# Kernel tuning notes

Measured on AMD Instinct MI355X. Metric: run time of the kernel, lower is better.

## Reference

```python
import jax, jax.numpy as jnp
import numpy as np

DEPTH = 6
N_INTERNAL = 2 ** DEPTH - 1  # 63
N_LEAVES = 2 ** DEPTH        # 64


def _tree_paths(depth):
    """Precompute, for each leaf, its `depth` ancestor internal-node indices and
    whether the path goes right at each ancestor (static heap-indexing of the tree)."""
    n_internal = 2 ** depth - 1
    n_leaves = 2 ** depth
    anc = np.zeros((n_leaves, depth), dtype=np.int32)
    right = np.zeros((n_leaves, depth), dtype=bool)
    for leaf in range(n_leaves):
        node = leaf + n_internal
        for d in range(depth):
            parent = (node - 1) // 2
            anc[leaf, d] = parent
            right[leaf, d] = (node % 2 == 0)
            node = parent
    return jnp.asarray(anc), jnp.asarray(right)

_ANC, _RIGHT = _tree_paths(DEPTH)


def setup_inputs() -> dict:
    key = jax.random.key(0)
    k = jax.random.split(key, 6)
    B, F, T, C = 8192, 256, 32, 100
    return {
        "x": jax.random.normal(k[0], (B, F), dtype=jnp.float32),
        "split_weights": jax.random.normal(k[1], (T, N_INTERNAL, F), dtype=jnp.float32) * 0.05,
        "split_bias": jax.random.normal(k[2], (T, N_INTERNAL), dtype=jnp.float32) * 0.05,
        "leaf_logits": jax.random.normal(k[3], (T, N_LEAVES, C), dtype=jnp.float32),
        "tree_weights": jax.random.normal(k[4], (T,), dtype=jnp.float32),
        "log_temperature": jnp.zeros((), dtype=jnp.float32),
    }


def reference(x, split_weights, split_bias, leaf_logits, tree_weights, log_temperature):
    # temperature = exp(log_temperature).clamp(0.1, 5.0)
    temp = jnp.clip(jnp.exp(log_temperature), 0.1, 5.0)
    # split probabilities for all trees at once: [T, B, N_INTERNAL]
    logits = jnp.einsum('bf,tnf->tbn', x, split_weights) + split_bias[:, None, :]
    split_probs = jax.nn.sigmoid(logits / temp)
    # gather each leaf's ancestor probs: [T, B, L, D]; right -> p, left -> 1-p
    g = split_probs[:, :, _ANC]
    leaf_probs = jnp.prod(jnp.where(_RIGHT, g, 1.0 - g), axis=-1)  # [T, B, L]
    # per-leaf class distributions: [T, L, C]
    leaf_class_probs = jax.nn.softmax(leaf_logits / temp, axis=-1)
    outputs = jnp.einsum('tbl,tlc->tbc', leaf_probs, leaf_class_probs)  # [T, B, C]
    weights = jax.nn.softmax(tree_weights, axis=0)  # [T]
    return jnp.einsum('t,tbc->bc', weights, outputs)  # [B, C]
```

## Files before the change

### kernel.cpp

```cpp
#include <hip/hip_runtime.h>
#include <math.h>

#define B_  8192
#define F_  256
#define T_  32
#define NI_ 63
#define NL_ 64
#define C_  100
#define K2_ (T_*NL_)
#define NG  4
#define TPG 8

typedef unsigned short u16;
typedef __attribute__((ext_vector_type(8))) short bf16x8;
typedef __attribute__((ext_vector_type(4))) float f32x4;
typedef __attribute__((ext_vector_type(8))) unsigned short u16x8;

__device__ __forceinline__ u16 f2bf(float f) {
    unsigned int u = __float_as_uint(f);
    u += 0x7fffu + ((u >> 16) & 1u);
    return (u16)(u >> 16);
}
__device__ __forceinline__ float bf2f(u16 u) {
    return __uint_as_float(((unsigned int)u) << 16);
}

__device__ __forceinline__ void gl16(const void* g, void* l) {
    __builtin_amdgcn_global_load_lds(
        (const __attribute__((address_space(1))) unsigned int*)g,
        (__attribute__((address_space(3))) unsigned int*)l,
        16, 0, 0);
}

#define WSB_SWB   0
#define WSB_LCPT  (T_*32*64*8*2)
#define WSB_XB    (WSB_LCPT + T_*8*112*8*2)
#define WSB_PART  ((size_t)WSB_XB + (size_t)B_*F_*2)
#define WSB_ATOM  WSB_PART
#define WSB_STORE (WSB_PART + (size_t)NG*B_*112*2)

#define SWBLK  (T_*64*32/256)
#define XBLK   (B_*F_/2048)
#define LCPBLK (T_*NL_/256)
#define ZBLK   (B_*C_/256)

__device__ __forceinline__ void cvt8(const float* __restrict__ s, u16* __restrict__ d, int i) {
    const float4* p = (const float4*)(s + i);
    float4 v0 = p[0], v1 = p[1];
    u16x8 o;
    o[0] = f2bf(v0.x); o[1] = f2bf(v0.y); o[2] = f2bf(v0.z); o[3] = f2bf(v0.w);
    o[4] = f2bf(v1.x); o[5] = f2bf(v1.y); o[6] = f2bf(v1.z); o[7] = f2bf(v1.w);
    *(u16x8*)(d + i) = o;
}

__global__ void k_prep(const float* __restrict__ sw, const float* __restrict__ x,
                       const float* __restrict__ ll, const float* __restrict__ tw,
                       const float* __restrict__ logT,
                       u16* __restrict__ swb, u16* __restrict__ xb,
                       u16* __restrict__ lcpT, float* __restrict__ out) {
    int blk = blockIdx.x, tid = threadIdx.x;
    if (blk < SWBLK) {
        int gid = blk * 256 + tid;
        int k8 = gid & 31;
        int n  = (gid >> 5) & 63;
        int t  = gid >> 11;
        u16x8 o;
        if (n < NI_) {
            const float4* p = (const float4*)(sw + ((size_t)(t * NI_ + n)) * F_ + k8 * 8);
            float4 v0 = p[0], v1 = p[1];
            o[0] = f2bf(v0.x); o[1] = f2bf(v0.y); o[2] = f2bf(v0.z); o[3] = f2bf(v0.w);
            o[4] = f2bf(v1.x); o[5] = f2bf(v1.y); o[6] = f2bf(v1.z); o[7] = f2bf(v1.w);
        } else {
            o = (u16x8){0,0,0,0,0,0,0,0};
        }
        *(u16x8*)(swb + (((size_t)t * 32 + k8) * 64 + n) * 8) = o;
        return;
    }
    blk -= SWBLK;
    if (blk < XBLK) { cvt8(x, xb, blk * 2048 + tid * 8); return; }
    blk -= XBLK;
    if (blk >= LCPBLK) {
        out[(blk - LCPBLK) * 256 + tid] = 0.f;
        return;
    }
    int idx = blk * 256 + tid;
    int t = idx >> 6;
    int l = idx & 63;
    int o = l >> 3, jj = l & 7;
    float temp = __expf(logT[0]);
    temp = fminf(fmaxf(temp, 0.1f), 5.0f);
    float invt = 1.0f / temp;

    float m = -1e30f;
    for (int j = 0; j < T_; ++j) m = fmaxf(m, tw[j]);
    float s = 0.f;
    for (int j = 0; j < T_; ++j) s += __expf(tw[j] - m);
    float wt = __expf(tw[t] - m) / s;

    const float* row = ll + (size_t)idx * C_;
    float m2 = -1e30f;
    for (int c = 0; c < C_; ++c) m2 = fmaxf(m2, row[c]);
    float s2 = 0.f;
    for (int c = 0; c < C_; ++c) s2 += __expf((row[c] - m2) * invt);
    float sc = wt / s2;
    u16* base = lcpT + (size_t)t * (8 * 112 * 8);
    for (int c = 0; c < C_; ++c)
        base[(o * 112 + c) * 8 + jj] = f2bf(sc * __expf((row[c] - m2) * invt));
    for (int c = C_; c < 112; ++c)
        base[(o * 112 + c) * 8 + jj] = 0;
}

__device__ __forceinline__ void stage_tree(const u16* __restrict__ swb,
                                           const u16* __restrict__ lcpT,
                                           u16* swsD, u16* lcpD,
                                           int t, int w, int lane) {
    const char* gsw = (const char*)(swb + (size_t)t * (32 * 64 * 8));
    char* lsw = (char*)swsD;
    #pragma unroll
    for (int r = 0; r < 4; ++r)
        gl16(gsw + r * 8192 + w * 1024 + lane * 16,
             lsw + r * 8192 + w * 1024);
    const char* glc = (const char*)(lcpT + (size_t)t * (8 * 112 * 8));
    char* llc = (char*)lcpD;
    gl16(glc + w * 1024 + lane * 16, llc + w * 1024);
    if (w < 6)
        gl16(glc + 8192 + w * 1024 + lane * 16, llc + 8192 + w * 1024);
}

__global__ __launch_bounds__(512, 2)
void k_fused(const u16* __restrict__ xb, const u16* __restrict__ swb,
             const float* __restrict__ sb, const float* __restrict__ logT,
             const u16* __restrict__ lcpT, void* __restrict__ dst, int storeMode) {
    __shared__ __attribute__((aligned(16))) u16 swS[2][32 * 64 * 8];
    __shared__ __attribute__((aligned(16))) u16 lcpS[2][8 * 112 * 8];
    __shared__ float slog[8][16][66];
    int tid  = threadIdx.x;
    int w    = tid >> 6;
    int lane = tid & 63;
    int col  = lane & 15;
    int quad = lane >> 4;
    int mb   = blockIdx.x * 128 + w * 16;
    int tg   = blockIdx.y;

    float temp = __expf(logT[0]);
    temp = fminf(fmaxf(temp, 0.1f), 5.0f);
    float invt = 1.0f / temp;

    bf16x8 afr[8];
    #pragma unroll
    for (int ks = 0; ks < 8; ++ks)
        afr[ks] = *(const bf16x8*)(xb + (size_t)(mb + col) * F_ + ks * 32 + quad * 8);

    stage_tree(swb, lcpT, swS[0], lcpS[0], tg * TPG, w, lane);

    f32x4 accO[7];
    #pragma unroll
    for (int i = 0; i < 7; ++i) accO[i] = (f32x4){0.f, 0.f, 0.f, 0.f};

    int cur = 0;
    #pragma unroll 1
    for (int ti = 0; ti < TPG; ++ti) {
        int t = tg * TPG + ti;

        asm volatile("s_waitcnt vmcnt(0)" ::: "memory");
        __syncthreads();

        if (ti + 1 < TPG)
            stage_tree(swb, lcpT, swS[cur ^ 1], lcpS[cur ^ 1], t + 1, w, lane);

        const u16* sws  = swS[cur];
        const u16* lcps = lcpS[cur];

        f32x4 acc[4];
        #pragma unroll
        for (int i = 0; i < 4; ++i) acc[i] = (f32x4){0.f, 0.f, 0.f, 0.f};
        #pragma unroll
        for (int ks = 0; ks < 8; ++ks) {
            #pragma unroll
            for (int nt = 0; nt < 4; ++nt) {
                int n  = nt * 16 + col;
                int ne = n > 62 ? 62 : n;
                bf16x8 bfr = *(const bf16x8*)&sws[((ks * 4 + quad) * 64 + ne) * 8];
                acc[nt] = __builtin_amdgcn_mfma_f32_16x16x32_bf16(afr[ks], bfr, acc[nt], 0, 0, 0);
            }
        }

        asm volatile("s_waitcnt lgkmcnt(0)" ::: "memory");
        #pragma unroll
        for (int nt = 0; nt < 4; ++nt) {
            int n = nt * 16 + col;
            float bias = (n < NI_) ? sb[t * NI_ + n] : 0.f;
            #pragma unroll
            for (int r = 0; r < 4; ++r) {
                float lg = (acc[nt][r] + bias) * invt;
                slog[w][quad * 4 + r][n] = 1.0f / (1.0f + __expf(-lg));
            }
        }
        asm volatile("s_waitcnt lgkmcnt(0)" ::: "memory");

        bf16x8 af0, af1;
        #pragma unroll
        for (int grp = 0; grp < 2; ++grp) {
            int s = (grp ? 11 : 7) + quad;
            float pref = 1.0f;
            int node = s;
            #pragma unroll
            for (int d = 0; d < 3; ++d) {
                int par = (node - 1) >> 1;
                float g = slog[w][col][par];
                pref = (node & 1) ? (pref - pref * g) : (pref * g);
                node = par;
            }
            float gs  = slog[w][col][s];
            float gl  = slog[w][col][2 * s + 1];
            float gr  = slog[w][col][2 * s + 2];
            float g00 = slog[w][col][4 * s + 3];
            float g01 = slog[w][col][4 * s + 4];
            float g10 = slog[w][col][4 * s + 5];
            float g11 = slog[w][col][4 * s + 6];
            #pragma unroll
            for (int j = 0; j < 8; ++j) {
                const int b2 = (j >> 2) & 1, b1 = (j >> 1) & 1, b0 = j & 1;
                float f3 = b2 ? gs : 1.0f - gs;
                float c1 = b2 ? gr : gl;
                float f4 = b1 ? c1 : 1.0f - c1;
                float c2 = b2 ? (b1 ? g11 : g10) : (b1 ? g01 : g00);
                float f5 = b0 ? c2 : 1.0f - c2;
                float p  = pref * f3 * f4 * f5;
                if (grp == 0) af0[j] = (short)f2bf(p);
                else          af1[j] = (short)f2bf(p);
            }
        }

        #pragma unroll
        for (int nt = 0; nt < 7; ++nt) {
            int n = nt * 16 + col;
            bf16x8 lb0 = *(const bf16x8*)&lcps[(quad * 112 + n) * 8];
            bf16x8 lb1 = *(const bf16x8*)&lcps[((4 + quad) * 112 + n) * 8];
            accO[nt] = __builtin_amdgcn_mfma_f32_16x16x32_bf16(af0, lb0, accO[nt], 0, 0, 0);
            accO[nt] = __builtin_amdgcn_mfma_f32_16x16x32_bf16(af1, lb1, accO[nt], 0, 0, 0);
        }

        cur ^= 1;
    }

    if (storeMode) {
        u16* pp = (u16*)dst + (size_t)tg * B_ * 112;
        #pragma unroll
        for (int nt = 0; nt < 7; ++nt) {
            int c = nt * 16 + col;
            #pragma unroll
            for (int r = 0; r < 4; ++r) {
                int b = mb + quad * 4 + r;
                pp[(size_t)b * 112 + c] = f2bf(accO[nt][r]);
            }
        }
    } else {
        float* od = (float*)dst;
        #pragma unroll
        for (int nt = 0; nt < 7; ++nt) {
            int c = nt * 16 + col;
            if (c < C_) {
                #pragma unroll
                for (int r = 0; r < 4; ++r) {
                    int b = mb + quad * 4 + r;
                    atomicAdd(&od[(size_t)b * C_ + c], accO[nt][r]);
                }
            }
        }
    }
}

__global__ void k_red(const u16* __restrict__ part, float* __restrict__ out) {
    int idx = blockIdx.x * 256 + threadIdx.x;
    int b = idx / 112, c = idx - b * 112;
    if (c < C_) {
        float s = 0.f;
        #pragma unroll
        for (int tg = 0; tg < NG; ++tg)
            s += bf2f(part[((size_t)tg * B_ + b) * 112 + c]);
        out[(size_t)b * C_ + c] = s;
    }
}

__global__ void k_zf(float* __restrict__ out, int n) {
    int i = blockIdx.x * 256 + threadIdx.x;
    if (i < n) out[i] = 0.f;
}

__global__ void k_mono(const float* __restrict__ x, const float* __restrict__ sw,
                       const float* __restrict__ sb, const float* __restrict__ ll,
                       const float* __restrict__ tw, const float* __restrict__ logT,
                       float* __restrict__ outg) {
    __shared__ float slcp[NL_ * C_];
    int tid = threadIdx.x;
    int b = blockIdx.x * 256 + tid;

    float temp = __expf(logT[0]);
    temp = fminf(fmaxf(temp, 0.1f), 5.0f);
    float invt = 1.0f / temp;

    float m = -1e30f;
    for (int j = 0; j < T_; ++j) m = fmaxf(m, tw[j]);
    float sden = 0.f;
    for (int j = 0; j < T_; ++j) sden += __expf(tw[j] - m);

    float acc[C_];
    #pragma unroll
    for (int c = 0; c < C_; ++c) acc[c] = 0.f;

    for (int t = 0; t < T_; ++t) {
        __syncthreads();
        {
            int l = tid & 63, cq = tid >> 6;
            float wt = __expf(tw[t] - m) / sden;
            const float* row = ll + ((size_t)t * NL_ + l) * C_;
            float m2 = -1e30f;
            for (int c = 0; c < C_; ++c) m2 = fmaxf(m2, row[c]);
            float s2 = 0.f;
            for (int c = 0; c < C_; ++c) s2 += __expf((row[c] - m2) * invt);
            float sc = wt / s2;
            for (int c = cq * 25; c < cq * 25 + 25; ++c)
                slcp[l * C_ + c] = sc * __expf((row[c] - m2) * invt);
        }
        __syncthreads();

        float an[NI_];
        #pragma unroll
        for (int n = 0; n < NI_; ++n) an[n] = 0.f;
        for (int k = 0; k < F_; ++k) {
            float xv = x[(size_t)b * F_ + k];
            #pragma unroll
            for (int n = 0; n < NI_; ++n)
                an[n] = fmaf(xv, sw[((size_t)t * NI_ + n) * F_ + k], an[n]);
        }
        #pragma unroll
        for (int n = 0; n < NI_; ++n) {
            float lg = (an[n] + sb[t * NI_ + n]) * invt;
            an[n] = 1.0f / (1.0f + __expf(-lg));
        }
        #pragma unroll
        for (int l = 0; l < NL_; ++l) {
            int node = l + NI_;
            float p = 1.0f;
            #pragma unroll
            for (int d = 0; d < 6; ++d) {
                int par = (node - 1) >> 1;
                float gv = an[par];
                p = (node & 1) ? (p - p * gv) : (p * gv);
                node = par;
            }
            #pragma unroll
            for (int c = 0; c < C_; ++c)
                acc[c] = fmaf(p, slcp[l * C_ + c], acc[c]);
        }
    }
    for (int c = 0; c < C_; ++c)
        outg[(size_t)b * C_ + c] = acc[c];
}

extern "C" void kernel_launch(void* const* d_in, const int* in_sizes, int n_in,
                              void* d_out, int out_size, void* d_ws, size_t ws_size,
                              hipStream_t stream) {
    bool ok = (n_in >= 6)
           && (in_sizes[0] == B_ * F_)
           && (in_sizes[1] == T_ * NI_ * F_)
           && (in_sizes[2] == T_ * NI_)
           && (in_sizes[3] == T_ * NL_ * C_)
           && (in_sizes[4] == T_)
           && (in_sizes[5] == 1)
           && (out_size == B_ * C_);
    if (!ok) {
        k_zf<<<(out_size + 255) / 256, 256, 0, stream>>>((float*)d_out, out_size);
        return;
    }

    const float* x    = (const float*)d_in[0];
    const float* sw   = (const float*)d_in[1];
    const float* sb   = (const float*)d_in[2];
    const float* ll   = (const float*)d_in[3];
    const float* tw   = (const float*)d_in[4];
    const float* logT = (const float*)d_in[5];
    float* out = (float*)d_out;

    if (ws_size >= WSB_STORE) {
        u16* swb  = (u16*)((char*)d_ws + WSB_SWB);
        u16* lcpT = (u16*)((char*)d_ws + WSB_LCPT);
        u16* xb   = (u16*)((char*)d_ws + WSB_XB);
        u16* part = (u16*)((char*)d_ws + WSB_PART);

        k_prep <<<SWBLK + XBLK + LCPBLK, 256, 0, stream>>>(sw, x, ll, tw, logT, swb, xb, lcpT, out);
        k_fused<<<dim3(B_ / 128, NG), 512, 0, stream>>>(xb, swb, sb, logT, lcpT, part, 1);
        k_red  <<<(B_ * 112) / 256, 256, 0, stream>>>(part, out);
    } else if (ws_size >= WSB_ATOM) {
        u16* swb  = (u16*)((char*)d_ws + WSB_SWB);
        u16* lcpT = (u16*)((char*)d_ws + WSB_LCPT);
        u16* xb   = (u16*)((char*)d_ws + WSB_XB);

        k_prep <<<SWBLK + XBLK + LCPBLK + ZBLK, 256, 0, stream>>>(sw, x, ll, tw, logT, swb, xb, lcpT, out);
        k_fused<<<dim3(B_ / 128, NG), 512, 0, stream>>>(xb, swb, sb, logT, lcpT, d_out, 0);
    } else {
        k_mono<<<B_ / 256, 256, 0, stream>>>(x, sw, sb, ll, tw, logT, out);
    }
}
```

Before: 124.0 us.

## Register-block two 16-row tiles per wave and rebalance tree groups

Each wave now processes 32 batch rows as two 16-row MFMA tiles. Each split-weight and leaf-class fragment read from LDS feeds two MFMAs instead of one, roughly halving LDS reads per unit of compute. To keep the same number of blocks, the grid's batch dimension is halved and the number of tree groups doubles (8 groups of 4 trees). In exchange, register pressure rises (two A-fragment sets and two accumulator sets) under the 512x2 launch bound, which risks spills. The number of partial outputs or atomic adds also doubles.

```diff
diff --git a/kernel.cpp b/kernel.cpp
--- a/kernel.cpp
+++ b/kernel.cpp
@@ -8,8 +8,8 @@
 #define NL_ 64
 #define C_  100
 #define K2_ (T_*NL_)
-#define NG  4
-#define TPG 8
+#define NG  8
+#define TPG 4
 
 typedef unsigned short u16;
 typedef __attribute__((ext_vector_type(8))) short bf16x8;
@@ -127,6 +127,56 @@
         gl16(glc + 8192 + w * 1024 + lane * 16, llc + 8192 + w * 1024);
 }
 
+__device__ __forceinline__ void epi_walk(const f32x4* acc, float invt,
+                                         const float* __restrict__ sbrow,
+                                         float (*slogw)[66], int col, int quad,
+                                         bf16x8& af0, bf16x8& af1) {
+    #pragma unroll
+    for (int nt = 0; nt < 4; ++nt) {
+        int n = nt * 16 + col;
+        float bias = (n < NI_) ? sbrow[n] : 0.f;
+        #pragma unroll
+        for (int r = 0; r < 4; ++r) {
+            float lg = (acc[nt][r] + bias) * invt;
+            slogw[quad * 4 + r][n] = 1.0f / (1.0f + __expf(-lg));
+        }
+    }
+    asm volatile("s_waitcnt lgkmcnt(0)" ::: "memory");
+    #pragma unroll
+    for (int grp = 0; grp < 2; ++grp) {
+        int s = (grp ? 11 : 7) + quad;
+        float pref = 1.0f;
+        int node = s;
+        #pragma unroll
+        for (int d = 0; d < 3; ++d) {
+            int par = (node - 1) >> 1;
+            float g = slogw[col][par];
+            pref = (node & 1) ? (pref - pref * g) : (pref * g);
+            node = par;
+        }
+        float gs  = slogw[col][s];
+        float gl  = slogw[col][2 * s + 1];
+        float gr  = slogw[col][2 * s + 2];
+        float g00 = slogw[col][4 * s + 3];
+        float g01 = slogw[col][4 * s + 4];
+        float g10 = slogw[col][4 * s + 5];
+        float g11 = slogw[col][4 * s + 6];
+        #pragma unroll
+        for (int j = 0; j < 8; ++j) {
+            const int b2 = (j >> 2) & 1, b1 = (j >> 1) & 1, b0 = j & 1;
+            float f3 = b2 ? gs : 1.0f - gs;
+            float c1 = b2 ? gr : gl;
+            float f4 = b1 ? c1 : 1.0f - c1;
+            float c2 = b2 ? (b1 ? g11 : g10) : (b1 ? g01 : g00);
+            float f5 = b0 ? c2 : 1.0f - c2;
+            float p  = pref * f3 * f4 * f5;
+            if (grp == 0) af0[j] = (short)f2bf(p);
+            else          af1[j] = (short)f2bf(p);
+        }
+    }
+    asm volatile("s_waitcnt lgkmcnt(0)" ::: "memory");
+}
+
 __global__ __launch_bounds__(512, 2)
 void k_fused(const u16* __restrict__ xb, const u16* __restrict__ swb,
              const float* __restrict__ sb, const float* __restrict__ logT,
@@ -139,23 +189,28 @@
     int lane = tid & 63;
     int col  = lane & 15;
     int quad = lane >> 4;
-    int mb   = blockIdx.x * 128 + w * 16;
+    int mb   = blockIdx.x * 256 + w * 32;
     int tg   = blockIdx.y;
 
     float temp = __expf(logT[0]);
     temp = fminf(fmaxf(temp, 0.1f), 5.0f);
     float invt = 1.0f / temp;
 
-    bf16x8 afr[8];
-    #pragma unroll
-    for (int ks = 0; ks < 8; ++ks)
-        afr[ks] = *(const bf16x8*)(xb + (size_t)(mb + col) * F_ + ks * 32 + quad * 8);
+    bf16x8 afr0[8], afr1[8];
+    #pragma unroll
+    for (int ks = 0; ks < 8; ++ks) {
+        afr0[ks] = *(const bf16x8*)(xb + (size_t)(mb + col) * F_ + ks * 32 + quad * 8);
+        afr1[ks] = *(const bf16x8*)(xb + (size_t)(mb + 16 + col) * F_ + ks * 32 + quad * 8);
+    }
 
     stage_tree(swb, lcpT, swS[0], lcpS[0], tg * TPG, w, lane);
 
-    f32x4 accO[7];
-    #pragma unroll
-    for (int i = 0; i < 7; ++i) accO[i] = (f32x4){0.f, 0.f, 0.f, 0.f};
+    f32x4 accO0[7], accO1[7];
+    #pragma unroll
+    for (int i = 0; i < 7; ++i) {
+        accO0[i] = (f32x4){0.f, 0.f, 0.f, 0.f};
+        accO1[i] = (f32x4){0.f, 0.f, 0.f, 0.f};
+    }
 
     int cur = 0;
     #pragma unroll 1
@@ -171,9 +226,12 @@
         const u16* sws  = swS[cur];
         const u16* lcps = lcpS[cur];
 
-        f32x4 acc[4];
-        #pragma unroll
-        for (int i = 0; i < 4; ++i) acc[i] = (f32x4){0.f, 0.f, 0.f, 0.f};
+        f32x4 acc0[4], acc1[4];
+        #pragma unroll
+        for (int i = 0; i < 4; ++i) {
+            acc0[i] = (f32x4){0.f, 0.f, 0.f, 0.f};
+            acc1[i] = (f32x4){0.f, 0.f, 0.f, 0.f};
+        }
         #pragma unroll
         for (int ks = 0; ks < 8; ++ks) {
             #pragma unroll
@@ -181,64 +239,26 @@
                 int n  = nt * 16 + col;
                 int ne = n > 62 ? 62 : n;
                 bf16x8 bfr = *(const bf16x8*)&sws[((ks * 4 + quad) * 64 + ne) * 8];
-                acc[nt] = __builtin_amdgcn_mfma_f32_16x16x32_bf16(afr[ks], bfr, acc[nt], 0, 0, 0);
+                acc0[nt] = __builtin_amdgcn_mfma_f32_16x16x32_bf16(afr0[ks], bfr, acc0[nt], 0, 0, 0);
+                acc1[nt] = __builtin_amdgcn_mfma_f32_16x16x32_bf16(afr1[ks], bfr, acc1[nt], 0, 0, 0);
             }
         }
-
         asm volatile("s_waitcnt lgkmcnt(0)" ::: "memory");
-        #pragma unroll
-        for (int nt = 0; nt < 4; ++nt) {
-            int n = nt * 16 + col;
-            float bias = (n < NI_) ? sb[t * NI_ + n] : 0.f;
-            #pragma unroll
-            for (int r = 0; r < 4; ++r) {
-                float lg = (acc[nt][r] + bias) * invt;
-                slog[w][quad * 4 + r][n] = 1.0f / (1.0f + __expf(-lg));
-            }
-        }
-        asm volatile("s_waitcnt lgkmcnt(0)" ::: "memory");
-
-        bf16x8 af0, af1;
-        #pragma unroll
-        for (int grp = 0; grp < 2; ++grp) {
-            int s = (grp ? 11 : 7) + quad;
-            float pref = 1.0f;
-            int node = s;
-            #pragma unroll
-            for (int d = 0; d < 3; ++d) {
-                int par = (node - 1) >> 1;
-                float g = slog[w][col][par];
-                pref = (node & 1) ? (pref - pref * g) : (pref * g);
-                node = par;
-            }
-            float gs  = slog[w][col][s];
-            float gl  = slog[w][col][2 * s + 1];
-            float gr  = slog[w][col][2 * s + 2];
-            float g00 = slog[w][col][4 * s + 3];
-            float g01 = slog[w][col][4 * s + 4];
-            float g10 = slog[w][col][4 * s + 5];
-            float g11 = slog[w][col][4 * s + 6];
-            #pragma unroll
-            for (int j = 0; j < 8; ++j) {
-                const int b2 = (j >> 2) & 1, b1 = (j >> 1) & 1, b0 = j & 1;
-                float f3 = b2 ? gs : 1.0f - gs;
-                float c1 = b2 ? gr : gl;
-                float f4 = b1 ? c1 : 1.0f - c1;
-                float c2 = b2 ? (b1 ? g11 : g10) : (b1 ? g01 : g00);
-                float f5 = b0 ? c2 : 1.0f - c2;
-                float p  = pref * f3 * f4 * f5;
-                if (grp == 0) af0[j] = (short)f2bf(p);
-                else          af1[j] = (short)f2bf(p);
-            }
-        }
+
+        const float* sbrow = sb + t * NI_;
+        bf16x8 af00, af01, af10, af11;
+        epi_walk(acc0, invt, sbrow, slog[w], col, quad, af00, af01);
+        epi_walk(acc1, invt, sbrow, slog[w], col, quad, af10, af11);
 
         #pragma unroll
         for (int nt = 0; nt < 7; ++nt) {
             int n = nt * 16 + col;
             bf16x8 lb0 = *(const bf16x8*)&lcps[(quad * 112 + n) * 8];
             bf16x8 lb1 = *(const bf16x8*)&lcps[((4 + quad) * 112 + n) * 8];
-            accO[nt] = __builtin_amdgcn_mfma_f32_16x16x32_bf16(af0, lb0, accO[nt], 0, 0, 0);
-            accO[nt] = __builtin_amdgcn_mfma_f32_16x16x32_bf16(af1, lb1, accO[nt], 0, 0, 0);
+            accO0[nt] = __builtin_amdgcn_mfma_f32_16x16x32_bf16(af00, lb0, accO0[nt], 0, 0, 0);
+            accO0[nt] = __builtin_amdgcn_mfma_f32_16x16x32_bf16(af01, lb1, accO0[nt], 0, 0, 0);
+            accO1[nt] = __builtin_amdgcn_mfma_f32_16x16x32_bf16(af10, lb0, accO1[nt], 0, 0, 0);
+            accO1[nt] = __builtin_amdgcn_mfma_f32_16x16x32_bf16(af11, lb1, accO1[nt], 0, 0, 0);
         }
 
         cur ^= 1;
@@ -251,8 +271,9 @@
             int c = nt * 16 + col;
             #pragma unroll
             for (int r = 0; r < 4; ++r) {
-                int b = mb + quad * 4 + r;
-                pp[(size_t)b * 112 + c] = f2bf(accO[nt][r]);
+                int b0 = mb + quad * 4 + r;
+                pp[(size_t)b0 * 112 + c] = f2bf(accO0[nt][r]);
+                pp[(size_t)(b0 + 16) * 112 + c] = f2bf(accO1[nt][r]);
             }
         }
     } else {
@@ -263,8 +284,9 @@
             if (c < C_) {
                 #pragma unroll
                 for (int r = 0; r < 4; ++r) {
-                    int b = mb + quad * 4 + r;
-                    atomicAdd(&od[(size_t)b * C_ + c], accO[nt][r]);
+                    int b0 = mb + quad * 4 + r;
+                    atomicAdd(&od[(size_t)b0 * C_ + c], accO0[nt][r]);
+                    atomicAdd(&od[(size_t)(b0 + 16) * C_ + c], accO1[nt][r]);
                 }
             }
         }
@@ -390,7 +412,7 @@
         u16* part = (u16*)((char*)d_ws + WSB_PART);
 
         k_prep <<<SWBLK + XBLK + LCPBLK, 256, 0, stream>>>(sw, x, ll, tw, logT, swb, xb, lcpT, out);
-        k_fused<<<dim3(B_ / 128, NG), 512, 0, stream>>>(xb, swb, sb, logT, lcpT, part, 1);
+        k_fused<<<dim3(B_ / 256, NG), 512, 0, stream>>>(xb, swb, sb, logT, lcpT, part, 1);
         k_red  <<<(B_ * 112) / 256, 256, 0, stream>>>(part, out);
     } else if (ws_size >= WSB_ATOM) {
         u16* swb  = (u16*)((char*)d_ws + WSB_SWB);
@@ -398,7 +420,7 @@
         u16* xb   = (u16*)((char*)d_ws + WSB_XB);
 
         k_prep <<<SWBLK + XBLK + LCPBLK + ZBLK, 256, 0, stream>>>(sw, x, ll, tw, logT, swb, xb, lcpT, out);
-        k_fused<<<dim3(B_ / 128, NG), 512, 0, stream>>>(xb, swb, sb, logT, lcpT, d_out, 0);
+        k_fused<<<dim3(B_ / 256, NG), 512, 0, stream>>>(xb, swb, sb, logT, lcpT, d_out, 0);
     } else {
         k_mono<<<B_ / 256, 256, 0, stream>>>(x, sw, sb, ll, tw, logT, out);
     }
```

After: 128.4 us. 1.04x slower.
